# Optimization experiments

Hardware: AMD Instinct MI355X
Metric: run time of the kernel (lower is better)

Reference implementation:

```python
import jax, jax.numpy as jnp
import numpy as np

# Dimensions
B2, T, C = 400, 120, 128          # x: ((B*V), T, C)
V = 25                            # num_point (skeleton joints)
NH_A = 3                          # adjacency heads (A.shape[0])
HEADS, DH = 8, 64                 # attention heads, dim_head
INNER = HEADS * DH                # 512
QKV_C = INNER * 3                 # 1536 = GCN out_channels
EPS = 1e-5                        # torch BatchNorm2d default eps


def setup_inputs() -> dict:
    key = jax.random.key(0)
    ks = jax.random.split(key, 12)
    z = lambda *s: jnp.zeros(s, jnp.float32)
    o = lambda *s: jnp.ones(s, jnp.float32)
    return {
        "x": jax.random.normal(ks[0], (B2, T, C), jnp.float32),
        # GCN shared topology (num_head, V, V)
        "A": jax.random.normal(ks[1], (NH_A, V, V), jnp.float32) * 0.2,
        # per-head 1x1 conv weights/biases (stacked)
        "conv_w": jax.random.normal(ks[2], (NH_A, QKV_C, C), jnp.float32) * 0.02,
        "conv_b": jax.random.normal(ks[3], (NH_A, QKV_C), jnp.float32) * 0.01,
        # main BatchNorm2d (eval mode, running stats)
        "bn_gamma": jax.random.uniform(ks[4], (QKV_C,), jnp.float32, 0.5, 1.5),
        "bn_beta": z(QKV_C),
        "bn_mean": z(QKV_C),
        "bn_var": o(QKV_C),
        # down path: 1x1 conv + BatchNorm2d (in_c != out_c)
        "down_w": jax.random.normal(ks[5], (QKV_C, C), jnp.float32) * 0.02,
        "down_b": z(QKV_C),
        "dbn_gamma": jax.random.uniform(ks[6], (QKV_C,), jnp.float32, 0.5, 1.5),
        "dbn_beta": z(QKV_C),
        "dbn_mean": z(QKV_C),
        "dbn_var": o(QKV_C),
        # to_out Linear(inner_dim -> dim)
        "out_w": jax.random.normal(ks[7], (C, INNER), jnp.float32) * 0.02,
        "out_b": z(C),
    }


def _bn_eval(y, gamma, beta, mean, var):
    # y: (b, o, t, v); BN over channel axis 1, eval mode
    inv = gamma / jnp.sqrt(var + EPS)
    return y * inv[None, :, None, None] + (beta - mean * inv)[None, :, None, None]


def reference(x, A, conv_w, conv_b, bn_gamma, bn_beta, bn_mean, bn_var,
              down_w, down_b, dbn_gamma, dbn_beta, dbn_mean, dbn_var,
              out_w, out_b):
    B = B2 // V
    # '(b v) t c -> b c t v'
    x4 = x.reshape(B, V, T, C).transpose(0, 3, 2, 1)  # (b, c, t, v)

    # ---- GCN projection: sum_h Conv1x1_h(A_h @ x) ----
    z = jnp.einsum('hvu,bctu->bhctv', A, x4)                    # (b,h,c,t,v)
    y = jnp.einsum('hoc,bhctv->botv', conv_w, z)                # (b,O,t,v)
    y = y + conv_b.sum(0)[None, :, None, None]
    y = _bn_eval(y, bn_gamma, bn_beta, bn_mean, bn_var)

    d = jnp.einsum('oc,bctv->botv', down_w, x4) + down_b[None, :, None, None]
    d = _bn_eval(d, dbn_gamma, dbn_beta, dbn_mean, dbn_var)

    y = jax.nn.relu(y + d)                                      # (b,O,t,v)

    # ---- attention over time per (batch*joint) row ----
    qkv = y.transpose(0, 3, 2, 1).reshape(B2, T, QKV_C)         # '(b v) t c'
    q, k, v = jnp.split(qkv, 3, axis=-1)
    split_heads = lambda t: t.reshape(B2, T, HEADS, DH).transpose(0, 2, 1, 3)
    q, k, v = split_heads(q), split_heads(k), split_heads(v)

    dots = jnp.einsum('bhid,bhjd->bhij', q, k) * (DH ** -0.5)
    mask = jnp.tril(jnp.ones((T, T), bool))                     # causal mask
    dots = jnp.where(mask[None, None], dots, -jnp.inf)
    attn = jax.nn.softmax(dots, axis=-1)                        # (B2,H,T,T)

    o = jnp.einsum('bhij,bhjd->bhid', attn, v)
    o = o.transpose(0, 2, 1, 3).reshape(B2, T, INNER)
    out = o @ out_w.T + out_b                                   # (B2,T,C)
    return out, attn
```

## Files before the change

### kernel.cpp

```cpp
#include <hip/hip_runtime.h>


typedef __bf16 bf16;
typedef __bf16 bf16x8 __attribute__((ext_vector_type(8)));
typedef __bf16 bf16x4 __attribute__((ext_vector_type(4)));
typedef float  f32x4  __attribute__((ext_vector_type(4)));
typedef __attribute__((address_space(1))) const void* gptr1;
typedef __attribute__((address_space(3))) void*       lptr3;

#define GLL16(g, l) __builtin_amdgcn_global_load_lds((gptr1)(g), (lptr3)(l), 16, 0, 0)
#define MFMA16(a, b, c) __builtin_amdgcn_mfma_f32_16x16x32_bf16(a, b, c, 0, 0, 0)

__global__ __launch_bounds__(256) void build_weights(
    const float* __restrict__ conv_w, const float* __restrict__ conv_b,
    const float* __restrict__ g1, const float* __restrict__ be1,
    const float* __restrict__ mu1, const float* __restrict__ va1,
    const float* __restrict__ down_w, const float* __restrict__ down_b,
    const float* __restrict__ g2, const float* __restrict__ be2,
    const float* __restrict__ mu2, const float* __restrict__ va2,
    const float* __restrict__ out_w,
    bf16* __restrict__ wcat, bf16* __restrict__ wout, float* __restrict__ bias)
{
    int idx = blockIdx.x * 256 + threadIdx.x;
    if (idx < 1536 * 512) {
        int o = idx >> 9, k = idx & 511;
        float s, w;
        if (k < 384) {
            int h = k >> 7, c = k & 127;
            s = g1[o] * rsqrtf(va1[o] + 1e-5f);
            w = conv_w[(h * 1536 + o) * 128 + c];
        } else {
            s = g2[o] * rsqrtf(va2[o] + 1e-5f);
            w = down_w[o * 128 + (k - 384)];
        }
        wcat[idx] = (bf16)(w * s);
    }
    int i2 = idx - 1536 * 512;
    if (i2 >= 0 && i2 < 128 * 512) wout[i2] = (bf16)out_w[i2];
    int i3 = idx - (1536 * 512 + 128 * 512);
    if (i3 >= 0 && i3 < 1536) {
        int o = i3;
        float s1 = g1[o] * rsqrtf(va1[o] + 1e-5f);
        float s2 = g2[o] * rsqrtf(va2[o] + 1e-5f);
        float cb = conv_b[o] + conv_b[1536 + o] + conv_b[2 * 1536 + o];
        bias[o] = cb * s1 + be1[o] - mu1[o] * s1
                + down_b[o] * s2 + be2[o] - mu2[o] * s2;
    }
}

__global__ __launch_bounds__(256) void transform(
    const float* __restrict__ x, const float* __restrict__ A,
    bf16* __restrict__ zt)
{
    __shared__ float xs[25][128];
    const int tid = threadIdx.x;
    const int bt = blockIdx.x;
    const int b = bt / 120, t = bt - b * 120;
    for (int i = tid; i < 25 * 128; i += 256) {
        int u = i >> 7, c = i & 127;
        xs[u][c] = x[((size_t)(b * 25 + u) * 120 + t) * 128 + c];
    }
    __syncthreads();
    const int c = tid & 127, g = tid >> 7;
    float xr[25];
    #pragma unroll
    for (int u = 0; u < 25; u++) xr[u] = xs[u][c];
    for (int idx = g; idx < 75; idx += 2) {
        int h = idx / 25, v = idx - h * 25;
        const float* Ap = A + (h * 25 + v) * 25;
        float acc = 0.f;
        #pragma unroll
        for (int u = 0; u < 25; u++) acc += Ap[u] * xr[u];
        zt[((size_t)(b * 25 + v) * 120 + t) * 512 + h * 128 + c] = (bf16)acc;
    }
    for (int v = g; v < 25; v += 2)
        zt[((size_t)(b * 25 + v) * 120 + t) * 512 + 384 + c] = (bf16)xs[v][c];
}

__global__ __launch_bounds__(256) void gemm_qkv(
    const bf16* __restrict__ wcat, const bf16* __restrict__ zt,
    const float* __restrict__ bias,
    bf16* __restrict__ qg, bf16* __restrict__ kg, bf16* __restrict__ vtg)
{
    __shared__ __align__(16) char smem[49152];
    const int tid = threadIdx.x, lane = tid & 63, wv = tid >> 6;
    const int wrow = wv >> 1, wcol = wv & 1;
    const int NB = 4500, q8 = NB >> 3, r8 = NB & 7;
    const int xcd = blockIdx.x & 7, sidx = blockIdx.x >> 3;
    const int vid = (xcd < r8 ? xcd * (q8 + 1) : r8 * (q8 + 1) + (xcd - r8) * q8) + sidx;
    const int mt = vid % 12, nt = vid / 12;
    const int colb = lane & 15, rg = lane >> 4;

    f32x4 zz = {0.f, 0.f, 0.f, 0.f};
    f32x4 acc[4][4];
    #pragma unroll
    for (int i = 0; i < 4; i++)
        #pragma unroll
        for (int j = 0; j < 4; j++) acc[i][j] = zz;

    const char* gA = (const char*)wcat + (size_t)mt * 128 * 1024;
    const char* gB = (const char*)zt + (size_t)nt * 128 * 1024;
    const int srow = lane >> 2;
    const int skb = (((lane & 3) ^ ((lane >> 3) & 3)) * 16);
    const int rgs = rg ^ ((colb >> 1) & 3);
    const int aoff0 = (wrow * 64 + colb) * 64 + rgs * 16;
    const int boff0 = (wcol * 64 + colb) * 64 + rgs * 16;

    #define STAGE_QKV(kt, b) do {                                              \
        char* As_ = smem + (b) * 16384; char* Bs_ = As_ + 8192;                \
        _Pragma("unroll")                                                      \
        for (int j = 0; j < 2; j++) {                                          \
            int ck = wv * 2 + j;  int row = ck * 16 + srow;                    \
            GLL16(gA + (size_t)row * 1024 + (kt) * 64 + skb, As_ + ck * 1024); \
            GLL16(gB + (size_t)row * 1024 + (kt) * 64 + skb, Bs_ + ck * 1024); \
        } } while (0)

    STAGE_QKV(0, 0);
    STAGE_QKV(1, 1);
    asm volatile("s_waitcnt vmcnt(4)" ::: "memory");
    __builtin_amdgcn_s_barrier();
    for (int kt = 0; kt < 16; kt++) {
        const char* As = smem + (kt % 3) * 16384;
        const char* Bs = As + 8192;
        bf16x8 af[4], bfr[4];
        #pragma unroll
        for (int m = 0; m < 4; m++)
            af[m] = *(const bf16x8*)(As + aoff0 + m * 1024);
        #pragma unroll
        for (int n = 0; n < 4; n++)
            bfr[n] = *(const bf16x8*)(Bs + boff0 + n * 1024);
        int kn = kt + 2;
        STAGE_QKV(kn < 16 ? kn : 15, kn % 3);
        __builtin_amdgcn_s_setprio(1);
        #pragma unroll
        for (int m = 0; m < 4; m++)
            #pragma unroll
            for (int n = 0; n < 4; n++)
                acc[m][n] = MFMA16(af[m], bfr[n], acc[m][n]);
        __builtin_amdgcn_s_setprio(0);
        asm volatile("s_waitcnt vmcnt(4)" ::: "memory");
        __builtin_amdgcn_s_barrier();
    }
    __builtin_amdgcn_sched_barrier(0);

    const int mtb = mt * 128, ntb = nt * 128;
    const int which = mtb >> 9;

    if (which < 2) {
        bf16* Lt = (bf16*)smem;
        const float qs = (which == 0) ? 0.125f : 1.0f;
        #pragma unroll
        for (int m = 0; m < 4; m++) {
            int o0 = wrow * 64 + m * 16 + rg * 4;
            float b0 = bias[mtb + o0 + 0], b1 = bias[mtb + o0 + 1];
            float b2 = bias[mtb + o0 + 2], b3 = bias[mtb + o0 + 3];
            #pragma unroll
            for (int nn = 0; nn < 4; nn++) {
                int n_ = wcol * 64 + nn * 16 + colb;
                bf16x4 pk;
                pk[0] = (bf16)(fmaxf(acc[m][nn][0] + b0, 0.f) * qs);
                pk[1] = (bf16)(fmaxf(acc[m][nn][1] + b1, 0.f) * qs);
                pk[2] = (bf16)(fmaxf(acc[m][nn][2] + b2, 0.f) * qs);
                pk[3] = (bf16)(fmaxf(acc[m][nn][3] + b3, 0.f) * qs);
                *(bf16x4*)((char*)Lt + n_ * 256 + ((o0 * 2) ^ ((n_ & 7) << 4))) = pk;
            }
        }
        __syncthreads();
        bf16* dst = (which == 0) ? qg : kg;
        #pragma unroll
        for (int i = 0; i < 8; i++) {
            int ch = i * 256 + tid;
            int n_ = ch >> 4, c16 = ch & 15;
            int ng = ntb + n_;
            int grp = ng / 120, t = ng - grp * 120;
            int o = mtb + c16 * 8;
            int hd = (o >> 6) & 7, dd0 = o & 63;
            bf16x8 vv = *(const bf16x8*)((const char*)Lt + n_ * 256 +
                                         ((c16 * 16) ^ ((n_ & 7) << 4)));
            *(bf16x8*)(dst + ((size_t)(grp * 8 + hd) * 120 + t) * 64 + dd0) = vv;
        }
    } else {
        #pragma unroll
        for (int m = 0; m < 4; m++) {
            #pragma unroll
            for (int reg = 0; reg < 4; reg++) {
                int o = mtb + wrow * 64 + m * 16 + rg * 4 + reg;
                float bo = bias[o];
                int hd = (o >> 6) & 7, dd = o & 63;
                #pragma unroll
                for (int nn = 0; nn < 4; nn++) {
                    int n = ntb + wcol * 64 + nn * 16 + colb;
                    int grp = n / 120, t = n - grp * 120;
                    float val = fmaxf(acc[m][nn][reg] + bo, 0.f);
                    vtg[((size_t)(grp * 8 + hd) * 64 + dd) * 128 + t] = (bf16)val;
                }
            }
        }
    }
    #undef STAGE_QKV
}

__global__ __launch_bounds__(256) void attn_k(
    const bf16* __restrict__ qg, const bf16* __restrict__ kg,
    const bf16* __restrict__ vtg, float* __restrict__ attn_out,
    bf16* __restrict__ og)
{
    __shared__ __align__(16) char sm[49152];
    char* Vt = sm;
    char* Ks = sm + 16384;
    char* Ps = sm + 16384;
    const int tid = threadIdx.x, lane = tid & 63, wv = tid >> 6;
    const int bh = blockIdx.x;
    const int colb = lane & 15, rg = lane >> 4;

    const char* ksrc = (const char*)kg + (size_t)bh * 15360;
    const char* vsrc = (const char*)vtg + (size_t)bh * 16384;
    #pragma unroll
    for (int is = 0; is < 4; is++) {
        int cb = is * 256 + wv * 64;
        if (cb < 960) {
            int bb = (cb + lane) * 16;
            int row = bb >> 7;
            int gsrc = (bb & ~127) | ((bb & 127) ^ ((row & 7) << 4));
            GLL16(ksrc + gsrc, Ks + cb * 16);
        }
        {
            int bb = (cb + lane) * 16;
            int row = bb >> 8;
            int gsrc = (bb & ~255) | ((bb & 255) ^ ((row & 7) << 4));
            GLL16(vsrc + gsrc, Vt + cb * 16);
        }
    }
    const char* qsrc = (const char*)qg + (size_t)bh * 15360;
    bf16x8 qf[2][2];
    #pragma unroll
    for (int kk = 0; kk < 2; kk++)
        #pragma unroll
        for (int m = 0; m < 2; m++) {
            int row = wv * 32 + m * 16 + colb;
            qf[kk][m] = *(const bf16x8*)(qsrc + (size_t)row * 128 + rg * 16 + kk * 64);
        }
    asm volatile("s_waitcnt vmcnt(0)" ::: "memory");
    __syncthreads();
    {
        f32x4 z = {0.f, 0.f, 0.f, 0.f};
        if (tid < 64) {
            int r = 120 + (tid >> 3), off = (tid & 7) * 16;
            *(f32x4*)(Ks + r * 128 + off) = z;
        } else if (tid < 128) {
            int d = tid - 64;
            *(f32x4*)(Vt + d * 256 + (240 ^ ((d & 7) << 4))) = z;
        }
    }
    __syncthreads();

    f32x4 accs[2][8];
    #pragma unroll
    for (int m = 0; m < 2; m++)
        #pragma unroll
        for (int ct = 0; ct < 8; ct++) accs[m][ct] = (f32x4){0.f, 0.f, 0.f, 0.f};
    #pragma unroll
    for (int kk = 0; kk < 2; kk++) {
        #pragma unroll
        for (int ct = 0; ct < 8; ct++) {
            int rk = ct * 16 + colb;
            int byo = rk * 128 + ((rg * 16 + kk * 64) ^ ((rk & 7) << 4));
            bf16x8 bk = *(const bf16x8*)(Ks + byo);
            accs[0][ct] = MFMA16(qf[kk][0], bk, accs[0][ct]);
            accs[1][ct] = MFMA16(qf[kk][1], bk, accs[1][ct]);
        }
    }
    __syncthreads();

    const int rqb = wv * 32;
    float* attn_base = attn_out + (size_t)bh * 120 * 120;
    #pragma unroll
    for (int m = 0; m < 2; m++) {
        #pragma unroll
        for (int reg = 0; reg < 4; reg++) {
            int t_q = rqb + m * 16 + rg * 4 + reg;
            float s[8], mx = -1e30f;
            #pragma unroll
            for (int ct = 0; ct < 8; ct++) {
                int col = ct * 16 + colb;
                bool valid = (col <= t_q) && (col < 120);
                s[ct] = valid ? accs[m][ct][reg] : -1e30f;
                mx = fmaxf(mx, s[ct]);
            }
            #pragma unroll
            for (int d = 1; d < 16; d <<= 1) mx = fmaxf(mx, __shfl_xor(mx, d, 64));
            float p[8], sum = 0.f;
            #pragma unroll
            for (int ct = 0; ct < 8; ct++) {
                p[ct] = (s[ct] > -1e29f) ? __expf(s[ct] - mx) : 0.f;
                sum += p[ct];
            }
            #pragma unroll
            for (int d = 1; d < 16; d <<= 1) sum += __shfl_xor(sum, d, 64);
            float inv = 1.f / sum;
            if (t_q < 120) {
                float* orow = attn_base + (size_t)t_q * 120;
                #pragma unroll
                for (int ct = 0; ct < 8; ct++) {
                    int col = ct * 16 + colb;
                    if (col < 120) orow[col] = p[ct] * inv;
                }
            }
            #pragma unroll
            for (int ct = 0; ct < 8; ct++) {
                int col = ct * 16 + colb;
                int byo = t_q * 256 + ((col * 2) ^ ((t_q & 7) << 4));
                *(bf16*)(Ps + byo) = (bf16)(p[ct] * inv);
            }
        }
    }
    __syncthreads();

    f32x4 acco[2][4];
    #pragma unroll
    for (int m = 0; m < 2; m++)
        #pragma unroll
        for (int dt = 0; dt < 4; dt++) acco[m][dt] = (f32x4){0.f, 0.f, 0.f, 0.f};
    for (int kk = 0; kk <= wv; kk++) {
        bf16x8 ap[2];
        #pragma unroll
        for (int m = 0; m < 2; m++) {
            int row = rqb + m * 16 + colb;
            int byo = row * 256 + ((rg * 16 + kk * 64) ^ ((row & 7) << 4));
            ap[m] = *(const bf16x8*)(Ps + byo);
        }
        #pragma unroll
        for (int dt = 0; dt < 4; dt++) {
            int rd = dt * 16 + colb;
            int byo = rd * 256 + ((rg * 16 + kk * 64) ^ ((rd & 7) << 4));
            bf16x8 bv = *(const bf16x8*)(Vt + byo);
            acco[0][dt] = MFMA16(ap[0], bv, acco[0][dt]);
            acco[1][dt] = MFMA16(ap[1], bv, acco[1][dt]);
        }
    }
    const int b2 = bh >> 3, h = bh & 7;
    #pragma unroll
    for (int m = 0; m < 2; m++)
        #pragma unroll
        for (int dt = 0; dt < 4; dt++)
            #pragma unroll
            for (int reg = 0; reg < 4; reg++) {
                int t = rqb + m * 16 + rg * 4 + reg;
                if (t < 120) {
                    int dfull = h * 64 + dt * 16 + colb;
                    og[((size_t)b2 * 120 + t) * 512 + dfull] = (bf16)acco[m][dt][reg];
                }
            }
}

__global__ __launch_bounds__(256) void gemm_out_k(
    const bf16* __restrict__ og, const bf16* __restrict__ wout,
    const float* __restrict__ outb, float* __restrict__ out)
{
    __shared__ __align__(16) char smem[49152];
    const int tid = threadIdx.x, lane = tid & 63, wv = tid >> 6;
    const int wrow = wv >> 1, wcol = wv & 1;
    const int nt = blockIdx.x;
    const int colb = lane & 15, rg = lane >> 4;

    f32x4 zz = {0.f, 0.f, 0.f, 0.f};
    f32x4 acc[4][4];
    #pragma unroll
    for (int i = 0; i < 4; i++)
        #pragma unroll
        for (int j = 0; j < 4; j++) acc[i][j] = zz;

    const char* gA = (const char*)og + (size_t)nt * 128 * 1024;
    const char* gB = (const char*)wout;
    const int srow = lane >> 2;
    const int skb = (((lane & 3) ^ ((lane >> 3) & 3)) * 16);
    const int rgs = rg ^ ((colb >> 1) & 3);
    const int aoff0 = (wrow * 64 + colb) * 64 + rgs * 16;
    const int boff0 = (wcol * 64 + colb) * 64 + rgs * 16;

    #define STAGE_OUT(kt, b) do {                                              \
        char* As_ = smem + (b) * 16384; char* Bs_ = As_ + 8192;                \
        _Pragma("unroll")                                                      \
        for (int j = 0; j < 2; j++) {                                          \
            int ck = wv * 2 + j;  int row = ck * 16 + srow;                    \
            GLL16(gA + (size_t)row * 1024 + (kt) * 64 + skb, As_ + ck * 1024); \
            GLL16(gB + (size_t)row * 1024 + (kt) * 64 + skb, Bs_ + ck * 1024); \
        } } while (0)

    STAGE_OUT(0, 0);
    STAGE_OUT(1, 1);
    asm volatile("s_waitcnt vmcnt(4)" ::: "memory");
    __builtin_amdgcn_s_barrier();
    for (int kt = 0; kt < 16; kt++) {
        const char* As = smem + (kt % 3) * 16384;
        const char* Bs = As + 8192;
        bf16x8 af[4], bfr[4];
        #pragma unroll
        for (int m = 0; m < 4; m++)
            af[m] = *(const bf16x8*)(As + aoff0 + m * 1024);
        #pragma unroll
        for (int n = 0; n < 4; n++)
            bfr[n] = *(const bf16x8*)(Bs + boff0 + n * 1024);
        int kn = kt + 2;
        STAGE_OUT(kn < 16 ? kn : 15, kn % 3);
        __builtin_amdgcn_s_setprio(1);
        #pragma unroll
        for (int m = 0; m < 4; m++)
            #pragma unroll
            for (int n = 0; n < 4; n++)
                acc[m][n] = MFMA16(af[m], bfr[n], acc[m][n]);
        __builtin_amdgcn_s_setprio(0);
        asm volatile("s_waitcnt vmcnt(4)" ::: "memory");
        __builtin_amdgcn_s_barrier();
    }
    __builtin_amdgcn_sched_barrier(0);

    const int rbase = nt * 128 + wrow * 64;
    #pragma unroll
    for (int m = 0; m < 4; m++)
        #pragma unroll
        for (int reg = 0; reg < 4; reg++) {
            int r = rbase + m * 16 + rg * 4 + reg;
            #pragma unroll
            for (int nn = 0; nn < 4; nn++) {
                int c = wcol * 64 + nn * 16 + colb;
                out[(size_t)r * 128 + c] = acc[m][nn][reg] + outb[c];
            }
        }
    #undef STAGE_OUT
}

extern "C" void kernel_launch(void* const* d_in, const int* in_sizes, int n_in,
                              void* d_out, int out_size, void* d_ws, size_t ws_size,
                              hipStream_t stream)
{
    (void)in_sizes; (void)n_in; (void)out_size; (void)ws_size;
    const float* x      = (const float*)d_in[0];
    const float* A      = (const float*)d_in[1];
    const float* conv_w = (const float*)d_in[2];
    const float* conv_b = (const float*)d_in[3];
    const float* bn_g   = (const float*)d_in[4];
    const float* bn_b   = (const float*)d_in[5];
    const float* bn_m   = (const float*)d_in[6];
    const float* bn_v   = (const float*)d_in[7];
    const float* dw     = (const float*)d_in[8];
    const float* db     = (const float*)d_in[9];
    const float* dg     = (const float*)d_in[10];
    const float* dbb    = (const float*)d_in[11];
    const float* dm     = (const float*)d_in[12];
    const float* dvv    = (const float*)d_in[13];
    const float* out_w  = (const float*)d_in[14];
    const float* out_b  = (const float*)d_in[15];

    char* ws = (char*)d_ws;
    const size_t OFF_WCAT = 0;
    const size_t OFF_WOUT = 1572864;
    const size_t OFF_BIAS = 1703936;
    const size_t OFF_ZT   = 1710080;
    const size_t OFF_Q    = 50862080;
    const size_t OFF_K    = 100014080;
    const size_t OFF_VT   = 149166080;
    const size_t OFF_O    = OFF_ZT;

    bf16*  wcat = (bf16*)(ws + OFF_WCAT);
    bf16*  wout = (bf16*)(ws + OFF_WOUT);
    float* bias = (float*)(ws + OFF_BIAS);
    bf16*  zt   = (bf16*)(ws + OFF_ZT);
    bf16*  qg   = (bf16*)(ws + OFF_Q);
    bf16*  kg   = (bf16*)(ws + OFF_K);
    bf16*  vtg  = (bf16*)(ws + OFF_VT);
    bf16*  og   = (bf16*)(ws + OFF_O);
    float* outp = (float*)d_out;
    float* attn = outp + 6144000;

    build_weights<<<3334, 256, 0, stream>>>(conv_w, conv_b, bn_g, bn_b, bn_m, bn_v,
                                            dw, db, dg, dbb, dm, dvv, out_w,
                                            wcat, wout, bias);
    transform<<<1920, 256, 0, stream>>>(x, A, zt);
    gemm_qkv<<<4500, 256, 0, stream>>>(wcat, zt, bias, qg, kg, vtg);
    attn_k<<<3200, 256, 0, stream>>>(qg, kg, vtg, attn, og);
    gemm_out_k<<<375, 256, 0, stream>>>(og, wout, out_b, outp);
}
```

Before: 282.1 us.

## Enlarge QKV GEMM tile to 128x256 with zero-padded activations

The QKV projection GEMM now computes a 128x256 output tile per block instead of 128x128. Each wave owns all 128 rows and a 64-column slice, which doubles the MFMA work per staged A fragment and halves the block count. The N dimension is padded to a multiple of 256 by zero-filling extra zt rows in build_weights, and the workspace offsets shift to make room. The LDS footprint grows to 72KB with a new swizzle, and the accumulator doubles to 128 floats per lane, raising register pressure and cutting occupancy. Stores are now bounds-guarded.

```diff
diff --git a/kernel.cpp b/kernel.cpp
--- a/kernel.cpp
+++ b/kernel.cpp
@@ -19,7 +19,8 @@
     const float* __restrict__ g2, const float* __restrict__ be2,
     const float* __restrict__ mu2, const float* __restrict__ va2,
     const float* __restrict__ out_w,
-    bf16* __restrict__ wcat, bf16* __restrict__ wout, float* __restrict__ bias)
+    bf16* __restrict__ wcat, bf16* __restrict__ wout, float* __restrict__ bias,
+    bf16* __restrict__ zt)
 {
     int idx = blockIdx.x * 256 + threadIdx.x;
     if (idx < 1536 * 512) {
@@ -46,6 +47,9 @@
         bias[o] = cb * s1 + be1[o] - mu1[o] * s1
                 + down_b[o] * s2 + be2[o] - mu2[o] * s2;
     }
+    int i4 = idx - (1536 * 512 + 128 * 512 + 1536);
+    if (i4 >= 0 && i4 < 128 * 512)
+        zt[(size_t)48000 * 512 + i4] = (bf16)0.f;
 }
 
 __global__ __launch_bounds__(256) void transform(
@@ -77,127 +81,144 @@
         zt[((size_t)(b * 25 + v) * 120 + t) * 512 + 384 + c] = (bf16)xs[v][c];
 }
 
-__global__ __launch_bounds__(256) void gemm_qkv(
+__global__ __launch_bounds__(256, 2) void gemm_qkv(
     const bf16* __restrict__ wcat, const bf16* __restrict__ zt,
     const float* __restrict__ bias,
     bf16* __restrict__ qg, bf16* __restrict__ kg, bf16* __restrict__ vtg)
 {
-    __shared__ __align__(16) char smem[49152];
-    const int tid = threadIdx.x, lane = tid & 63, wv = tid >> 6;
-    const int wrow = wv >> 1, wcol = wv & 1;
-    const int NB = 4500, q8 = NB >> 3, r8 = NB & 7;
-    const int xcd = blockIdx.x & 7, sidx = blockIdx.x >> 3;
-    const int vid = (xcd < r8 ? xcd * (q8 + 1) : r8 * (q8 + 1) + (xcd - r8) * q8) + sidx;
+    __shared__ __align__(16) char smem[73728];
+    const int tid = threadIdx.x, lane = tid & 63, wc = tid >> 6;
+    const int colb = lane & 15, rg = lane >> 4;
+    const int vid = (blockIdx.x & 7) * 282 + (blockIdx.x >> 3);
     const int mt = vid % 12, nt = vid / 12;
-    const int colb = lane & 15, rg = lane >> 4;
-
-    f32x4 zz = {0.f, 0.f, 0.f, 0.f};
-    f32x4 acc[4][4];
-    #pragma unroll
-    for (int i = 0; i < 4; i++)
-        #pragma unroll
-        for (int j = 0; j < 4; j++) acc[i][j] = zz;
-
-    const char* gA = (const char*)wcat + (size_t)mt * 128 * 1024;
-    const char* gB = (const char*)zt + (size_t)nt * 128 * 1024;
-    const int srow = lane >> 2;
-    const int skb = (((lane & 3) ^ ((lane >> 3) & 3)) * 16);
-    const int rgs = rg ^ ((colb >> 1) & 3);
-    const int aoff0 = (wrow * 64 + colb) * 64 + rgs * 16;
-    const int boff0 = (wcol * 64 + colb) * 64 + rgs * 16;
-
-    #define STAGE_QKV(kt, b) do {                                              \
-        char* As_ = smem + (b) * 16384; char* Bs_ = As_ + 8192;                \
-        _Pragma("unroll")                                                      \
-        for (int j = 0; j < 2; j++) {                                          \
-            int ck = wv * 2 + j;  int row = ck * 16 + srow;                    \
-            GLL16(gA + (size_t)row * 1024 + (kt) * 64 + skb, As_ + ck * 1024); \
-            GLL16(gB + (size_t)row * 1024 + (kt) * 64 + skb, Bs_ + ck * 1024); \
+    const int mtb = mt * 128, ntb = nt * 256;
+
+    f32x4 acc[8][4];
+    #pragma unroll
+    for (int i = 0; i < 8; i++)
+        #pragma unroll
+        for (int j = 0; j < 4; j++) acc[i][j] = (f32x4){0.f, 0.f, 0.f, 0.f};
+
+    const char* gA = (const char*)wcat + (size_t)mtb * 1024;
+    const char* gB = (const char*)zt + (size_t)ntb * 1024;
+
+    int aoff[8], boff[4];
+    #pragma unroll
+    for (int mi = 0; mi < 8; mi++) {
+        int lr = mi * 16 + colb;
+        aoff[mi] = lr * 64 + ((rg ^ ((lr + (lr >> 2)) & 3)) << 4);
+    }
+    #pragma unroll
+    for (int ni = 0; ni < 4; ni++) {
+        int lr = wc * 64 + ni * 16 + colb;
+        boff[ni] = lr * 64 + ((rg ^ ((lr + (lr >> 2)) & 3)) << 4);
+    }
+
+    #define STG(kt, bsel) do {                                                  \
+        char* As_ = smem + (bsel) * 24576; char* Bs_ = As_ + 8192;              \
+        _Pragma("unroll")                                                       \
+        for (int j = 0; j < 2; j++) {                                           \
+            int cb = j * 256 + wc * 64;  int c = cb + lane;                     \
+            int r = c >> 2, sp = c & 3;                                         \
+            int sl = sp ^ ((r + (r >> 2)) & 3);                                 \
+            GLL16(gA + (size_t)r * 1024 + (kt) * 64 + sl * 16, As_ + cb * 16);  \
+        }                                                                       \
+        _Pragma("unroll")                                                       \
+        for (int j = 0; j < 4; j++) {                                           \
+            int cb = j * 256 + wc * 64;  int c = cb + lane;                     \
+            int r = c >> 2, sp = c & 3;                                         \
+            int sl = sp ^ ((r + (r >> 2)) & 3);                                 \
+            GLL16(gB + (size_t)r * 1024 + (kt) * 64 + sl * 16, Bs_ + cb * 16);  \
         } } while (0)
 
-    STAGE_QKV(0, 0);
-    STAGE_QKV(1, 1);
-    asm volatile("s_waitcnt vmcnt(4)" ::: "memory");
+    STG(0, 0);
+    STG(1, 1);
+    asm volatile("s_waitcnt vmcnt(6)" ::: "memory");
     __builtin_amdgcn_s_barrier();
     for (int kt = 0; kt < 16; kt++) {
-        const char* As = smem + (kt % 3) * 16384;
+        const char* As = smem + (kt % 3) * 24576;
         const char* Bs = As + 8192;
-        bf16x8 af[4], bfr[4];
-        #pragma unroll
-        for (int m = 0; m < 4; m++)
-            af[m] = *(const bf16x8*)(As + aoff0 + m * 1024);
-        #pragma unroll
-        for (int n = 0; n < 4; n++)
-            bfr[n] = *(const bf16x8*)(Bs + boff0 + n * 1024);
+        bf16x8 af[8], bfr[4];
+        #pragma unroll
+        for (int mi = 0; mi < 8; mi++)
+            af[mi] = *(const bf16x8*)(As + aoff[mi]);
+        #pragma unroll
+        for (int ni = 0; ni < 4; ni++)
+            bfr[ni] = *(const bf16x8*)(Bs + boff[ni]);
         int kn = kt + 2;
-        STAGE_QKV(kn < 16 ? kn : 15, kn % 3);
+        STG(kn < 16 ? kn : 15, kn % 3);
         __builtin_amdgcn_s_setprio(1);
         #pragma unroll
-        for (int m = 0; m < 4; m++)
-            #pragma unroll
-            for (int n = 0; n < 4; n++)
-                acc[m][n] = MFMA16(af[m], bfr[n], acc[m][n]);
+        for (int mi = 0; mi < 8; mi++)
+            #pragma unroll
+            for (int ni = 0; ni < 4; ni++)
+                acc[mi][ni] = MFMA16(af[mi], bfr[ni], acc[mi][ni]);
         __builtin_amdgcn_s_setprio(0);
-        asm volatile("s_waitcnt vmcnt(4)" ::: "memory");
+        asm volatile("s_waitcnt vmcnt(6)" ::: "memory");
         __builtin_amdgcn_s_barrier();
     }
     __builtin_amdgcn_sched_barrier(0);
-
-    const int mtb = mt * 128, ntb = nt * 128;
+    asm volatile("s_waitcnt vmcnt(0)" ::: "memory");
+    __builtin_amdgcn_s_barrier();
+
     const int which = mtb >> 9;
 
     if (which < 2) {
         bf16* Lt = (bf16*)smem;
         const float qs = (which == 0) ? 0.125f : 1.0f;
         #pragma unroll
-        for (int m = 0; m < 4; m++) {
-            int o0 = wrow * 64 + m * 16 + rg * 4;
+        for (int mi = 0; mi < 8; mi++) {
+            int o0 = mi * 16 + rg * 4;
             float b0 = bias[mtb + o0 + 0], b1 = bias[mtb + o0 + 1];
             float b2 = bias[mtb + o0 + 2], b3 = bias[mtb + o0 + 3];
             #pragma unroll
-            for (int nn = 0; nn < 4; nn++) {
-                int n_ = wcol * 64 + nn * 16 + colb;
+            for (int ni = 0; ni < 4; ni++) {
+                int n_ = wc * 64 + ni * 16 + colb;
                 bf16x4 pk;
-                pk[0] = (bf16)(fmaxf(acc[m][nn][0] + b0, 0.f) * qs);
-                pk[1] = (bf16)(fmaxf(acc[m][nn][1] + b1, 0.f) * qs);
-                pk[2] = (bf16)(fmaxf(acc[m][nn][2] + b2, 0.f) * qs);
-                pk[3] = (bf16)(fmaxf(acc[m][nn][3] + b3, 0.f) * qs);
+                pk[0] = (bf16)(fmaxf(acc[mi][ni][0] + b0, 0.f) * qs);
+                pk[1] = (bf16)(fmaxf(acc[mi][ni][1] + b1, 0.f) * qs);
+                pk[2] = (bf16)(fmaxf(acc[mi][ni][2] + b2, 0.f) * qs);
+                pk[3] = (bf16)(fmaxf(acc[mi][ni][3] + b3, 0.f) * qs);
                 *(bf16x4*)((char*)Lt + n_ * 256 + ((o0 * 2) ^ ((n_ & 7) << 4))) = pk;
             }
         }
         __syncthreads();
         bf16* dst = (which == 0) ? qg : kg;
         #pragma unroll
-        for (int i = 0; i < 8; i++) {
+        for (int i = 0; i < 16; i++) {
             int ch = i * 256 + tid;
             int n_ = ch >> 4, c16 = ch & 15;
             int ng = ntb + n_;
-            int grp = ng / 120, t = ng - grp * 120;
-            int o = mtb + c16 * 8;
-            int hd = (o >> 6) & 7, dd0 = o & 63;
-            bf16x8 vv = *(const bf16x8*)((const char*)Lt + n_ * 256 +
-                                         ((c16 * 16) ^ ((n_ & 7) << 4)));
-            *(bf16x8*)(dst + ((size_t)(grp * 8 + hd) * 120 + t) * 64 + dd0) = vv;
+            if (ng < 48000) {
+                int grp = ng / 120, t = ng - grp * 120;
+                int o = mtb + c16 * 8;
+                int hd = (o >> 6) & 7, dd0 = o & 63;
+                bf16x8 vv = *(const bf16x8*)((const char*)Lt + n_ * 256 +
+                                             ((c16 * 16) ^ ((n_ & 7) << 4)));
+                *(bf16x8*)(dst + ((size_t)(grp * 8 + hd) * 120 + t) * 64 + dd0) = vv;
+            }
         }
     } else {
         #pragma unroll
-        for (int m = 0; m < 4; m++) {
+        for (int mi = 0; mi < 8; mi++) {
             #pragma unroll
             for (int reg = 0; reg < 4; reg++) {
-                int o = mtb + wrow * 64 + m * 16 + rg * 4 + reg;
+                int o = mtb + mi * 16 + rg * 4 + reg;
                 float bo = bias[o];
                 int hd = (o >> 6) & 7, dd = o & 63;
                 #pragma unroll
-                for (int nn = 0; nn < 4; nn++) {
-                    int n = ntb + wcol * 64 + nn * 16 + colb;
-                    int grp = n / 120, t = n - grp * 120;
-                    float val = fmaxf(acc[m][nn][reg] + bo, 0.f);
-                    vtg[((size_t)(grp * 8 + hd) * 64 + dd) * 128 + t] = (bf16)val;
+                for (int ni = 0; ni < 4; ni++) {
+                    int n = ntb + wc * 64 + ni * 16 + colb;
+                    if (n < 48000) {
+                        int grp = n / 120, t = n - grp * 120;
+                        float val = fmaxf(acc[mi][ni][reg] + bo, 0.f);
+                        vtg[((size_t)(grp * 8 + hd) * 64 + dd) * 128 + t] = (bf16)val;
+                    }
                 }
             }
         }
     }
-    #undef STAGE_QKV
+    #undef STG
 }
 
 __global__ __launch_bounds__(256) void attn_k(
@@ -457,9 +478,9 @@
     const size_t OFF_WOUT = 1572864;
     const size_t OFF_BIAS = 1703936;
     const size_t OFF_ZT   = 1710080;
-    const size_t OFF_Q    = 50862080;
-    const size_t OFF_K    = 100014080;
-    const size_t OFF_VT   = 149166080;
+    const size_t OFF_Q    = 50993152;
+    const size_t OFF_K    = 100145152;
+    const size_t OFF_VT   = 149297152;
     const size_t OFF_O    = OFF_ZT;
 
     bf16*  wcat = (bf16*)(ws + OFF_WCAT);
@@ -473,11 +494,11 @@
     float* outp = (float*)d_out;
     float* attn = outp + 6144000;
 
-    build_weights<<<3334, 256, 0, stream>>>(conv_w, conv_b, bn_g, bn_b, bn_m, bn_v,
+    build_weights<<<3590, 256, 0, stream>>>(conv_w, conv_b, bn_g, bn_b, bn_m, bn_v,
                                             dw, db, dg, dbb, dm, dvv, out_w,
-                                            wcat, wout, bias);
+                                            wcat, wout, bias, zt);
     transform<<<1920, 256, 0, stream>>>(x, A, zt);
-    gemm_qkv<<<4500, 256, 0, stream>>>(wcat, zt, bias, qg, kg, vtg);
+    gemm_qkv<<<2256, 256, 0, stream>>>(wcat, zt, bias, qg, kg, vtg);
     attn_k<<<3200, 256, 0, stream>>>(qg, kg, vtg, attn, og);
     gemm_out_k<<<375, 256, 0, stream>>>(og, wout, out_b, outp);
 }
```

Measured after the change: 305.4 us. 8.3% more time.

## Coalesce attention-probability stores from LDS and overlap V load with QK

Applied to the files above, without the earlier changes.

Attention probabilities are now written to global memory after the PV stage by reading the bf16 P tile from LDS and emitting contiguous float4 stores, instead of scattered per-lane fp32 stores during softmax. The V tile load is issued after the Q loads and waited on only after the QK^T MFMAs, with finer-grained waitcnt/barrier pairs replacing __syncthreads. This targets uncoalesced writes of the large attn output and exposed load latency. The written probabilities are now bf16-rounded values cast back to fp32, which reduces output precision.

```diff
diff --git a/kernel.cpp b/kernel.cpp
--- a/kernel.cpp
+++ b/kernel.cpp
@@ -224,12 +224,6 @@
             int gsrc = (bb & ~127) | ((bb & 127) ^ ((row & 7) << 4));
             GLL16(ksrc + gsrc, Ks + cb * 16);
         }
-        {
-            int bb = (cb + lane) * 16;
-            int row = bb >> 8;
-            int gsrc = (bb & ~255) | ((bb & 255) ^ ((row & 7) << 4));
-            GLL16(vsrc + gsrc, Vt + cb * 16);
-        }
     }
     const char* qsrc = (const char*)qg + (size_t)bh * 15360;
     bf16x8 qf[2][2];
@@ -240,19 +234,23 @@
             int row = wv * 32 + m * 16 + colb;
             qf[kk][m] = *(const bf16x8*)(qsrc + (size_t)row * 128 + rg * 16 + kk * 64);
         }
-    asm volatile("s_waitcnt vmcnt(0)" ::: "memory");
-    __syncthreads();
-    {
+    #pragma unroll
+    for (int is = 0; is < 4; is++) {
+        int cb = is * 256 + wv * 64;
+        int bb = (cb + lane) * 16;
+        int row = bb >> 8;
+        int gsrc = (bb & ~255) | ((bb & 255) ^ ((row & 7) << 4));
+        GLL16(vsrc + gsrc, Vt + cb * 16);
+    }
+    asm volatile("s_waitcnt vmcnt(4)" ::: "memory");
+    __builtin_amdgcn_s_barrier();
+    if (tid < 64) {
         f32x4 z = {0.f, 0.f, 0.f, 0.f};
-        if (tid < 64) {
-            int r = 120 + (tid >> 3), off = (tid & 7) * 16;
-            *(f32x4*)(Ks + r * 128 + off) = z;
-        } else if (tid < 128) {
-            int d = tid - 64;
-            *(f32x4*)(Vt + d * 256 + (240 ^ ((d & 7) << 4))) = z;
-        }
-    }
-    __syncthreads();
+        int r = 120 + (tid >> 3), off = (tid & 7) * 16;
+        *(f32x4*)(Ks + r * 128 + off) = z;
+    }
+    asm volatile("s_waitcnt lgkmcnt(0)" ::: "memory");
+    __builtin_amdgcn_s_barrier();
 
     f32x4 accs[2][8];
     #pragma unroll
@@ -270,10 +268,15 @@
             accs[1][ct] = MFMA16(qf[kk][1], bk, accs[1][ct]);
         }
     }
-    __syncthreads();
+    asm volatile("s_waitcnt vmcnt(0)" ::: "memory");
+    __builtin_amdgcn_s_barrier();
+    if (tid >= 64 && tid < 128) {
+        int d = tid - 64;
+        f32x4 z = {0.f, 0.f, 0.f, 0.f};
+        *(f32x4*)(Vt + d * 256 + (240 ^ ((d & 7) << 4))) = z;
+    }
 
     const int rqb = wv * 32;
-    float* attn_base = attn_out + (size_t)bh * 120 * 120;
     #pragma unroll
     for (int m = 0; m < 2; m++) {
         #pragma unroll
@@ -298,14 +301,6 @@
             #pragma unroll
             for (int d = 1; d < 16; d <<= 1) sum += __shfl_xor(sum, d, 64);
             float inv = 1.f / sum;
-            if (t_q < 120) {
-                float* orow = attn_base + (size_t)t_q * 120;
-                #pragma unroll
-                for (int ct = 0; ct < 8; ct++) {
-                    int col = ct * 16 + colb;
-                    if (col < 120) orow[col] = p[ct] * inv;
-                }
-            }
             #pragma unroll
             for (int ct = 0; ct < 8; ct++) {
                 int col = ct * 16 + colb;
@@ -314,7 +309,8 @@
             }
         }
     }
-    __syncthreads();
+    asm volatile("s_waitcnt lgkmcnt(0)" ::: "memory");
+    __builtin_amdgcn_s_barrier();
 
     f32x4 acco[2][4];
     #pragma unroll
@@ -338,6 +334,23 @@
             acco[1][dt] = MFMA16(ap[1], bv, acco[1][dt]);
         }
     }
+
+    {
+        float* attn_base = attn_out + (size_t)bh * 14400;
+        #pragma unroll
+        for (int i = 0; i < 15; i++) {
+            int chunk = i * 256 + tid;
+            if (chunk < 3600) {
+                int r = chunk / 30, c4 = chunk - r * 30;
+                int byo = r * 256 + ((c4 * 8) ^ ((r & 7) << 4));
+                bf16x4 pv4 = *(const bf16x4*)(Ps + byo);
+                f32x4 o4 = { (float)pv4[0], (float)pv4[1],
+                             (float)pv4[2], (float)pv4[3] };
+                *(f32x4*)(attn_base + chunk * 4) = o4;
+            }
+        }
+    }
+
     const int b2 = bh >> 3, h = bh & 7;
     #pragma unroll
     for (int m = 0; m < 2; m++)
```

Result: faster. 273.0 us (-3.2%).
